# Performance work log

Hardware: AMD Instinct MI355X
Metric: run time of the kernel (lower is better)

Reference implementation:

```python
import jax, jax.numpy as jnp
import numpy as np

K = 3          # kernel_size (local window)
PAD = 1        # padding = (K-1)//2 -> 'same' output size
GROUPS = 8
C_OUT = 64


def _unfold3d(x, k):
    """x: [B,C,Dp,Hp,Wp] -> [B,C,D,H,W,kd,kh,kw] sliding windows (stride 1)."""
    B, C, Dp, Hp, Wp = x.shape
    D, H, W = Dp - k + 1, Hp - k + 1, Wp - k + 1
    idx_d = jnp.arange(D)[:, None] + jnp.arange(k)[None, :]
    idx_h = jnp.arange(H)[:, None] + jnp.arange(k)[None, :]
    idx_w = jnp.arange(W)[:, None] + jnp.arange(k)[None, :]
    x = x[:, :, idx_d]              # [B,C,D,kd,Hp,Wp]
    x = x[:, :, :, :, idx_h]        # [B,C,D,kd,H,kh,Wp]
    x = x[:, :, :, :, :, :, idx_w]  # [B,C,D,kd,H,kh,W,kw]
    return jnp.transpose(x, (0, 1, 2, 4, 6, 3, 5, 7))


def setup_inputs() -> dict:
    key = jax.random.key(0)
    ks = jax.random.split(key, 7)
    B, Cin, D, H, W = 1, 64, 16, 64, 64
    c3 = C_OUT // 3                 # 21
    rest = C_OUT - 2 * c3           # 22
    fan_out_scale = np.sqrt(2.0 / C_OUT)  # kaiming_normal fan_out, relu
    x = jax.random.normal(ks[0], (B, Cin, D, H, W), dtype=jnp.float32)
    w_q = jax.random.normal(ks[1], (C_OUT, Cin), dtype=jnp.float32) * fan_out_scale
    w_k = jax.random.normal(ks[2], (C_OUT, Cin), dtype=jnp.float32) * fan_out_scale
    w_v = jax.random.normal(ks[3], (C_OUT, Cin), dtype=jnp.float32) * fan_out_scale
    rel_d = jax.random.normal(ks[4], (c3, 1, 1, 1, K, 1, 1), dtype=jnp.float32)
    rel_h = jax.random.normal(ks[5], (c3, 1, 1, 1, 1, K, 1), dtype=jnp.float32)
    rel_w = jax.random.normal(ks[6], (rest, 1, 1, 1, 1, 1, K), dtype=jnp.float32)
    return {"x": x, "w_q": w_q, "w_k": w_k, "w_v": w_v,
            "rel_d": rel_d, "rel_h": rel_h, "rel_w": rel_w}


def reference(x, w_q, w_k, w_v, rel_d, rel_h, rel_w):
    B, Cin, D, H, W = x.shape
    cg = C_OUT // GROUPS
    c3 = C_OUT // 3
    # 1x1x1 convs (bias=False): plain channel mixing. conv(pad(x)) == pad(conv(x)).
    q = jnp.einsum('oc,bcdhw->bodhw', w_q, x)
    k = jnp.einsum('oc,bcdhw->bodhw', w_k, x)
    v = jnp.einsum('oc,bcdhw->bodhw', w_v, x)
    pad = [(0, 0), (0, 0), (PAD, PAD), (PAD, PAD), (PAD, PAD)]
    k = jnp.pad(k, pad)
    v = jnp.pad(v, pad)
    k_win = _unfold3d(k, K)   # [B,Co,D,H,W,kd,kh,kw]
    v_win = _unfold3d(v, K)
    # split relative position bias across channel thirds
    k_win = jnp.concatenate([
        k_win[:, :c3] + rel_d,
        k_win[:, c3:2 * c3] + rel_h,
        k_win[:, 2 * c3:] + rel_w,
    ], axis=1)
    Kv = K * K * K
    k_win = k_win.reshape(B, GROUPS, cg, D, H, W, Kv)
    v_win = v_win.reshape(B, GROUPS, cg, D, H, W, Kv)
    qg = q.reshape(B, GROUPS, cg, D, H, W, 1)
    attn = jax.nn.softmax(qg * k_win, axis=-1)
    out = jnp.einsum('bncdhwk,bncdhwk->bncdhw', attn, v_win)
    return out.reshape(B, C_OUT, D, H, W)
```

## Files before the change

### kernel.cpp

```cpp
#include <hip/hip_runtime.h>

#define SP    65536
#define DD    16
#define HH    64
#define WW    64
#define CIN   64
#define COUT  64

#define XPAD  68


__global__ __launch_bounds__(256) void proj(const float* __restrict__ x,
                                            const float* __restrict__ wq,
                                            const float* __restrict__ wk,
                                            const float* __restrict__ wv,
                                            float* __restrict__ q,
                                            float* __restrict__ k,
                                            float* __restrict__ v) {
    __shared__ float xl[CIN][XPAD];
    __shared__ float wl[COUT][XPAD];

    const int t  = threadIdx.x;
    const int p0 = blockIdx.x * 64;
    const int m  = blockIdx.y;

    const float* __restrict__ wsel = (m == 0) ? wq : (m == 1) ? wk : wv;
    float* __restrict__       osel = (m == 0) ? q  : (m == 1) ? k  : v;

#pragma unroll
    for (int i = 0; i < 4; ++i) {
        const int f = t + 256 * i;
        const int c = f >> 4, j = f & 15;
        *(float4*)(&xl[c][j * 4]) = *(const float4*)(x + c * SP + p0 + j * 4);
    }
#pragma unroll
    for (int i = 0; i < 4; ++i) {
        const int f = t + 256 * i;
        const int o = f >> 4, j = f & 15;
        *(float4*)(&wl[o][j * 4]) = *(const float4*)(wsel + o * CIN + j * 4);
    }
    __syncthreads();

    const int og    = t >> 4;
    const int pg    = t & 15;
    const int obase = og * 4;
    const int pbase = pg * 4;

    float acc[4][4] = {};
#pragma unroll
    for (int c4 = 0; c4 < CIN / 4; ++c4) {
        float4 w4[4], x4[4];
#pragma unroll
        for (int i = 0; i < 4; ++i)
            w4[i] = *(const float4*)(&wl[obase + i][c4 * 4]);
#pragma unroll
        for (int cc = 0; cc < 4; ++cc)
            x4[cc] = *(const float4*)(&xl[c4 * 4 + cc][pbase]);
#pragma unroll
        for (int i = 0; i < 4; ++i) {
            acc[i][0] = fmaf(w4[i].x, x4[0].x, acc[i][0]);
            acc[i][1] = fmaf(w4[i].x, x4[0].y, acc[i][1]);
            acc[i][2] = fmaf(w4[i].x, x4[0].z, acc[i][2]);
            acc[i][3] = fmaf(w4[i].x, x4[0].w, acc[i][3]);
            acc[i][0] = fmaf(w4[i].y, x4[1].x, acc[i][0]);
            acc[i][1] = fmaf(w4[i].y, x4[1].y, acc[i][1]);
            acc[i][2] = fmaf(w4[i].y, x4[1].z, acc[i][2]);
            acc[i][3] = fmaf(w4[i].y, x4[1].w, acc[i][3]);
            acc[i][0] = fmaf(w4[i].z, x4[2].x, acc[i][0]);
            acc[i][1] = fmaf(w4[i].z, x4[2].y, acc[i][1]);
            acc[i][2] = fmaf(w4[i].z, x4[2].z, acc[i][2]);
            acc[i][3] = fmaf(w4[i].z, x4[2].w, acc[i][3]);
            acc[i][0] = fmaf(w4[i].w, x4[3].x, acc[i][0]);
            acc[i][1] = fmaf(w4[i].w, x4[3].y, acc[i][1]);
            acc[i][2] = fmaf(w4[i].w, x4[3].z, acc[i][2]);
            acc[i][3] = fmaf(w4[i].w, x4[3].w, acc[i][3]);
        }
    }

#pragma unroll
    for (int i = 0; i < 4; ++i) {
        const float4 st = make_float4(acc[i][0], acc[i][1], acc[i][2], acc[i][3]);
        *(float4*)(osel + (obase + i) * SP + p0 + pbase) = st;
    }
}

__device__ __forceinline__ float dpp_shr1(float x) {
    return __int_as_float(__builtin_amdgcn_mov_dpp(__float_as_int(x), 0x111, 0xf, 0xf, true));
}
__device__ __forceinline__ float dpp_shl1(float x) {
    return __int_as_float(__builtin_amdgcn_mov_dpp(__float_as_int(x), 0x101, 0xf, 0xf, true));
}

template<int AXIS>
__device__ __forceinline__ void attn_compute(const float* __restrict__ kt,
                                             const float* __restrict__ vt,
                                             const float (&qs)[4][4],
                                             float r0, float r1, float r2,
                                             int wg, int h, int dg,
                                             float (&s)[4][4], float (&a)[4][4]) {
#pragma unroll 1
    for (int m = 0; m < 6; ++m) {
#pragma unroll 1
        for (int kh = 0; kh < 3; ++kh) {
            const int row = (dg * 4 + m) * 10 + (h + kh);
            const float4 km = *(const float4*)(kt + row * 64 + wg * 4);
            const float4 vm = *(const float4*)(vt + row * 64 + wg * 4);
            const float kl = dpp_shr1(km.w), kr = dpp_shl1(km.x);
            const float vl = dpp_shr1(vm.w), vr = dpp_shl1(vm.x);
            const float krow[6] = { kl, km.x, km.y, km.z, km.w, kr };
            const float vrow[6] = { vl, vm.x, vm.y, vm.z, vm.w, vr };

            const float rkh = (kh == 0) ? r0 : (kh == 1) ? r1 : r2;

#pragma unroll
            for (int di = 0; di < 4; ++di) {
                const int kd = m - di;
                if ((unsigned)kd < 3u) {
                    const float rdd = (kd == 0) ? r0 : (kd == 1) ? r1 : r2;
                    const float rr  = (AXIS == 0) ? rdd : (AXIS == 1) ? rkh : 0.f;
#pragma unroll
                    for (int wi = 0; wi < 4; ++wi) {
                        const float qv = qs[di][wi];
#pragma unroll
                        for (int kw = 0; kw < 3; ++kw) {
                            const float rc = (AXIS == 2)
                                           ? ((kw == 0) ? r0 : (kw == 1) ? r1 : r2)
                                           : rr;
                            const float e = __expf(qv * (krow[wi + kw] + rc));
                            s[di][wi] += e;
                            a[di][wi] = fmaf(e, vrow[wi + kw], a[di][wi]);
                        }
                    }
                }
            }
        }
    }
}

__global__ __launch_bounds__(256) void attn(const float* __restrict__ kbuf,
                                            const float* __restrict__ vbuf,
                                            const float* __restrict__ qbuf,
                                            const float* __restrict__ rel_d,
                                            const float* __restrict__ rel_h,
                                            const float* __restrict__ rel_w,
                                            float* __restrict__ out) {
    __shared__ float kt[100 * 64];
    __shared__ float vt[100 * 64];

    const int dt = blockIdx.x;
    const int ht = blockIdx.y;
    const int o  = blockIdx.z;

    const int d0 = dt * 8;
    const int h0 = ht * 8;
    const int t  = threadIdx.x;

    const float* __restrict__ kc = kbuf + o * SP;
    const float* __restrict__ vc = vbuf + o * SP;

#pragma unroll
    for (int i = 0; i < 13; ++i) {
        const int idx = t + 256 * i;
        if (idx < 3200) {
            const bool isv = idx >= 1600;
            const int rem  = isv ? idx - 1600 : idx;
            const int row  = rem >> 4;
            const int j    = rem & 15;
            const int dp   = row / 10;
            const int hp   = row - dp * 10;
            const int dpg  = d0 - 1 + dp;
            const int hpg  = h0 - 1 + hp;
            float4 val = make_float4(0.f, 0.f, 0.f, 0.f);
            if ((unsigned)dpg < (unsigned)DD && (unsigned)hpg < (unsigned)HH) {
                const float* src = (isv ? vc : kc) + (dpg * HH + hpg) * WW + j * 4;
                val = *(const float4*)src;
            }
            *(float4*)((isv ? vt : kt) + row * 64 + j * 4) = val;
        }
    }

    const int wg = t & 15;
    const int h  = (t >> 4) & 7;
    const int dg = t >> 7;

    float qs[4][4];
#pragma unroll
    for (int di = 0; di < 4; ++di) {
        const int dabs = d0 + dg * 4 + di;
        const float4 q4 = *(const float4*)(qbuf + o * SP + (dabs * HH + (h0 + h)) * WW + wg * 4);
        qs[di][0] = q4.x; qs[di][1] = q4.y; qs[di][2] = q4.z; qs[di][3] = q4.w;
    }

    __syncthreads();

    float s[4][4] = {};
    float a[4][4] = {};

    if (o < 21) {
        attn_compute<0>(kt, vt, qs, rel_d[o * 3 + 0], rel_d[o * 3 + 1], rel_d[o * 3 + 2],
                        wg, h, dg, s, a);
    } else if (o < 42) {
        const int b = o - 21;
        attn_compute<1>(kt, vt, qs, rel_h[b * 3 + 0], rel_h[b * 3 + 1], rel_h[b * 3 + 2],
                        wg, h, dg, s, a);
    } else {
        const int b = o - 42;
        attn_compute<2>(kt, vt, qs, rel_w[b * 3 + 0], rel_w[b * 3 + 1], rel_w[b * 3 + 2],
                        wg, h, dg, s, a);
    }

#pragma unroll
    for (int di = 0; di < 4; ++di) {
        const int dabs = d0 + dg * 4 + di;
        float4 ov;
        ov.x = a[di][0] * __builtin_amdgcn_rcpf(s[di][0]);
        ov.y = a[di][1] * __builtin_amdgcn_rcpf(s[di][1]);
        ov.z = a[di][2] * __builtin_amdgcn_rcpf(s[di][2]);
        ov.w = a[di][3] * __builtin_amdgcn_rcpf(s[di][3]);
        *(float4*)(out + o * SP + (dabs * HH + (h0 + h)) * WW + wg * 4) = ov;
    }
}

extern "C" void kernel_launch(void* const* d_in, const int* in_sizes, int n_in,
                              void* d_out, int out_size, void* d_ws, size_t ws_size,
                              hipStream_t stream) {
    const float* x     = (const float*)d_in[0];
    const float* w_q   = (const float*)d_in[1];
    const float* w_k   = (const float*)d_in[2];
    const float* w_v   = (const float*)d_in[3];
    const float* rel_d = (const float*)d_in[4];
    const float* rel_h = (const float*)d_in[5];
    const float* rel_w = (const float*)d_in[6];
    float* out = (float*)d_out;

    float* ws = (float*)d_ws;
    float* q  = ws;
    float* k  = ws + (size_t)COUT * SP;
    float* v  = ws + 2 * (size_t)COUT * SP;

    proj<<<dim3(SP / 64, 3), 256, 0, stream>>>(x, w_q, w_k, w_v, q, k, v);
    attn<<<dim3(2, 8, 64), 256, 0, stream>>>(k, v, q, rel_d, rel_h, rel_w, out);
}
```

Measured before the change: 128.7 us.

## Fuse q/k/v projections per block to load x tile once

The projection kernel now computes all three q/k/v projections within one block, reusing a single LDS-loaded x tile instead of launching a separate grid slice per projection. Each lane holds its pixel's 64 input channels in registers and reads weight rows as wave-uniform loads from global memory. This cuts redundant x reads to one pass, at the cost of a third as many blocks, higher register use and per-lane scalar stores.

```diff
diff --git a/kernel.cpp b/kernel.cpp
--- a/kernel.cpp
+++ b/kernel.cpp
@@ -18,14 +18,9 @@
                                             float* __restrict__ k,
                                             float* __restrict__ v) {
     __shared__ float xl[CIN][XPAD];
-    __shared__ float wl[COUT][XPAD];
 
     const int t  = threadIdx.x;
     const int p0 = blockIdx.x * 64;
-    const int m  = blockIdx.y;
-
-    const float* __restrict__ wsel = (m == 0) ? wq : (m == 1) ? wk : wv;
-    float* __restrict__       osel = (m == 0) ? q  : (m == 1) ? k  : v;
 
 #pragma unroll
     for (int i = 0; i < 4; ++i) {
@@ -33,54 +28,37 @@
         const int c = f >> 4, j = f & 15;
         *(float4*)(&xl[c][j * 4]) = *(const float4*)(x + c * SP + p0 + j * 4);
     }
-#pragma unroll
-    for (int i = 0; i < 4; ++i) {
-        const int f = t + 256 * i;
-        const int o = f >> 4, j = f & 15;
-        *(float4*)(&wl[o][j * 4]) = *(const float4*)(wsel + o * CIN + j * 4);
-    }
     __syncthreads();
 
-    const int og    = t >> 4;
-    const int pg    = t & 15;
-    const int obase = og * 4;
-    const int pbase = pg * 4;
-
-    float acc[4][4] = {};
-#pragma unroll
-    for (int c4 = 0; c4 < CIN / 4; ++c4) {
-        float4 w4[4], x4[4];
-#pragma unroll
-        for (int i = 0; i < 4; ++i)
-            w4[i] = *(const float4*)(&wl[obase + i][c4 * 4]);
-#pragma unroll
-        for (int cc = 0; cc < 4; ++cc)
-            x4[cc] = *(const float4*)(&xl[c4 * 4 + cc][pbase]);
-#pragma unroll
-        for (int i = 0; i < 4; ++i) {
-            acc[i][0] = fmaf(w4[i].x, x4[0].x, acc[i][0]);
-            acc[i][1] = fmaf(w4[i].x, x4[0].y, acc[i][1]);
-            acc[i][2] = fmaf(w4[i].x, x4[0].z, acc[i][2]);
-            acc[i][3] = fmaf(w4[i].x, x4[0].w, acc[i][3]);
-            acc[i][0] = fmaf(w4[i].y, x4[1].x, acc[i][0]);
-            acc[i][1] = fmaf(w4[i].y, x4[1].y, acc[i][1]);
-            acc[i][2] = fmaf(w4[i].y, x4[1].z, acc[i][2]);
-            acc[i][3] = fmaf(w4[i].y, x4[1].w, acc[i][3]);
-            acc[i][0] = fmaf(w4[i].z, x4[2].x, acc[i][0]);
-            acc[i][1] = fmaf(w4[i].z, x4[2].y, acc[i][1]);
-            acc[i][2] = fmaf(w4[i].z, x4[2].z, acc[i][2]);
-            acc[i][3] = fmaf(w4[i].z, x4[2].w, acc[i][3]);
-            acc[i][0] = fmaf(w4[i].w, x4[3].x, acc[i][0]);
-            acc[i][1] = fmaf(w4[i].w, x4[3].y, acc[i][1]);
-            acc[i][2] = fmaf(w4[i].w, x4[3].z, acc[i][2]);
-            acc[i][3] = fmaf(w4[i].w, x4[3].w, acc[i][3]);
+    const int lane  = t & 63;
+    const int wvid  = __builtin_amdgcn_readfirstlane(t >> 6);
+    const int obase = wvid * 16;
+
+    float xv[CIN];
+#pragma unroll
+    for (int c = 0; c < CIN; ++c)
+        xv[c] = xl[c][lane];
+
+#pragma unroll 1
+    for (int m = 0; m < 3; ++m) {
+        const float* __restrict__ wsel = (m == 0) ? wq : (m == 1) ? wk : wv;
+        float* __restrict__       osel = (m == 0) ? q  : (m == 1) ? k  : v;
+
+#pragma unroll 1
+        for (int oo = 0; oo < 16; ++oo) {
+            const int o = obase + oo;
+            const float* __restrict__ wrow = wsel + o * CIN;
+            float acc = 0.f;
+#pragma unroll
+            for (int c4 = 0; c4 < CIN / 4; ++c4) {
+                const float4 w4 = *(const float4*)(wrow + c4 * 4);
+                acc = fmaf(w4.x, xv[4 * c4 + 0], acc);
+                acc = fmaf(w4.y, xv[4 * c4 + 1], acc);
+                acc = fmaf(w4.z, xv[4 * c4 + 2], acc);
+                acc = fmaf(w4.w, xv[4 * c4 + 3], acc);
+            }
+            osel[o * SP + p0 + lane] = acc;
         }
-    }
-
-#pragma unroll
-    for (int i = 0; i < 4; ++i) {
-        const float4 st = make_float4(acc[i][0], acc[i][1], acc[i][2], acc[i][3]);
-        *(float4*)(osel + (obase + i) * SP + p0 + pbase) = st;
     }
 }
 
@@ -238,6 +216,6 @@
     float* k  = ws + (size_t)COUT * SP;
     float* v  = ws + 2 * (size_t)COUT * SP;
 
-    proj<<<dim3(SP / 64, 3), 256, 0, stream>>>(x, w_q, w_k, w_v, q, k, v);
+    proj<<<SP / 64, 256, 0, stream>>>(x, w_q, w_k, w_v, q, k, v);
     attn<<<dim3(2, 8, 64), 256, 0, stream>>>(k, v, q, rel_d, rel_h, rel_w, out);
 }
```

After: 187.0 us. +45.3%, slower.
